# Optimization experiments

Measured on AMD Instinct MI355X. Metric: run time of the kernel, lower is better.

Reference implementation:

```python
import jax, jax.numpy as jnp
import numpy as np

WS, SHIFT, HEADS = 8, 4, 12
B, H0, W0, C, HID = 16, 64, 64, 384, 1536
EPS = 1e-5


def _rel_pos_index():
    # WindowMSA.double_step_seq(2*Ww-1, Wh, 1, Ww), then coords + coords.T, then flip(1)
    seq1 = np.arange(0, (2 * WS - 1) * WS, 2 * WS - 1)
    seq2 = np.arange(0, WS)
    coords = (seq1[:, None] + seq2[None, :]).reshape(1, -1)  # (1, N)
    idx = coords + coords.T                                   # (N, N)
    return np.ascontiguousarray(idx[:, ::-1]).reshape(-1)

REL_IDX = jnp.asarray(_rel_pos_index())


def _attn_mask(Hp, Wp):
    # Swin shift mask: region labels -> per-window pairwise (-100 where regions differ)
    img = np.zeros((Hp, Wp))
    sl = (slice(0, -WS), slice(-WS, -SHIFT), slice(-SHIFT, None))
    cnt = 0
    for hs in sl:
        for ws in sl:
            img[hs, ws] = cnt
            cnt += 1
    mw = img.reshape(Hp // WS, WS, Wp // WS, WS).transpose(0, 2, 1, 3).reshape(-1, WS * WS)
    am = mw[:, None, :] - mw[:, :, None]
    return jnp.asarray(np.where(am != 0, -100.0, 0.0), np.float32)


def _ln(z, g, b):
    m = z.mean(-1, keepdims=True)
    v = ((z - m) ** 2).mean(-1, keepdims=True)
    return (z - m) * jax.lax.rsqrt(v + EPS) * g + b


def _bn(z, g, b):
    # eval-mode BatchNorm2d with running mean=0, var=1
    scale = g * (1.0 / np.sqrt(1.0 + EPS))
    return z * scale[None, :, None, None] + b[None, :, None, None]


def setup_inputs() -> dict:
    key = jax.random.key(0)
    ks = jax.random.split(key, 8)
    p = lambda k, sh: jax.random.normal(k, sh, jnp.float32) * 0.02
    return {
        "x": jax.random.normal(ks[0], (B, H0 * W0, C), jnp.float32),
        "H": H0, "W": W0,
        "ln1_g": jnp.ones((C,), jnp.float32), "ln1_b": jnp.zeros((C,), jnp.float32),
        "qkv_w": p(ks[1], (3 * C, C)), "qkv_b": jnp.zeros((3 * C,), jnp.float32),
        "rpb_table": p(ks[2], ((2 * WS - 1) ** 2, HEADS)),
        "proj_w": p(ks[3], (C, C)), "proj_b": jnp.zeros((C,), jnp.float32),
        "ln2_g": jnp.ones((C,), jnp.float32), "ln2_b": jnp.zeros((C,), jnp.float32),
        "fc1_w": p(ks[4], (HID, C)), "fc1_b": jnp.zeros((HID,), jnp.float32),
        "bn1_g": jnp.ones((HID,), jnp.float32), "bn1_b": jnp.zeros((HID,), jnp.float32),
        "dw_w": p(ks[5], (HID, 1, 3, 3)), "dw_b": jnp.zeros((HID,), jnp.float32),
        "bn2_g": jnp.ones((HID,), jnp.float32), "bn2_b": jnp.zeros((HID,), jnp.float32),
        "fc2_w": p(ks[6], (C, HID)), "fc2_b": jnp.zeros((C,), jnp.float32),
        "bn3_g": jnp.ones((C,), jnp.float32), "bn3_b": jnp.zeros((C,), jnp.float32),
    }


def reference(x, H, W, ln1_g, ln1_b, qkv_w, qkv_b, rpb_table, proj_w, proj_b,
              ln2_g, ln2_b, fc1_w, fc1_b, bn1_g, bn1_b, dw_w, dw_b,
              bn2_g, bn2_b, fc2_w, fc2_b, bn3_g, bn3_b):
    Bx, L, Cx = x.shape
    hd = Cx // HEADS
    # ---------- shifted-window MHSA branch ----------
    h = _ln(x, ln1_g, ln1_b).reshape(Bx, H, W, Cx)
    h = jnp.roll(h, (-SHIFT, -SHIFT), axis=(1, 2))
    nH, nW = H // WS, W // WS
    N = WS * WS
    win = h.reshape(Bx, nH, WS, nW, WS, Cx).transpose(0, 1, 3, 2, 4, 5).reshape(-1, N, Cx)
    qkv = (win @ qkv_w.T + qkv_b).reshape(-1, N, 3, HEADS, hd).transpose(2, 0, 3, 1, 4)
    q, k, v = qkv[0] * (hd ** -0.5), qkv[1], qkv[2]  # (B*nW, heads, N, hd)
    attn = jnp.einsum('whnd,whmd->whnm', q, k)
    bias = rpb_table[REL_IDX].reshape(N, N, HEADS).transpose(2, 0, 1)  # (heads, N, N)
    attn = attn + bias[None]
    mask = _attn_mask(H, W)  # (num_windows, N, N)
    attn = attn.reshape(Bx, nH * nW, HEADS, N, N) + mask[None, :, None]
    attn = jax.nn.softmax(attn.reshape(-1, HEADS, N, N), axis=-1)
    out = jnp.einsum('whnm,whmd->whnd', attn, v).transpose(0, 2, 1, 3).reshape(-1, N, Cx)
    out = out @ proj_w.T + proj_b
    out = out.reshape(Bx, nH, nW, WS, WS, Cx).transpose(0, 1, 3, 2, 4, 5).reshape(Bx, H, W, Cx)
    out = jnp.roll(out, (SHIFT, SHIFT), axis=(1, 2)).reshape(Bx, L, Cx)
    x = x + out
    # ---------- MlpDWBN branch ----------
    h = _ln(x, ln2_g, ln2_b)
    z = h.transpose(0, 2, 1).reshape(Bx, Cx, H, W)
    z = jnp.einsum('oc,bchw->bohw', fc1_w, z) + fc1_b[None, :, None, None]
    z = jax.nn.gelu(_bn(z, bn1_g, bn1_b), approximate=False)
    z = jax.lax.conv_general_dilated(z, dw_w, (1, 1), 'SAME',
                                     feature_group_count=z.shape[1],
                                     dimension_numbers=('NCHW', 'OIHW', 'NCHW'))
    z = z + dw_b[None, :, None, None]
    z = jax.nn.gelu(_bn(z, bn2_g, bn2_b), approximate=False)
    z = jnp.einsum('oc,bchw->bohw', fc2_w, z) + fc2_b[None, :, None, None]
    z = jax.nn.gelu(_bn(z, bn3_g, bn3_b), approximate=False)
    z = z.reshape(Bx, Cx, -1).transpose(0, 2, 1)
    return x + z
```

## Files before the change

### kernel.cpp

```cpp
#include <hip/hip_runtime.h>
#include <cstddef>


#define CCH 384
#define HIDCH 1536

typedef __attribute__((ext_vector_type(8))) short short8;
typedef __attribute__((ext_vector_type(4))) float f32x4;

__device__ __forceinline__ float gelu_exact(float v) {
  return 0.5f * v * (1.0f + erff(v * 0.70710678118654752440f));
}
__device__ __forceinline__ unsigned short f2bf(float f) {
  unsigned u = __builtin_bit_cast(unsigned, f);
  u = (u + 0x7FFF + ((u >> 16) & 1)) >> 16;
  return (unsigned short)u;
}
__device__ __forceinline__ float bf2f(unsigned short s) {
  return __builtin_bit_cast(float, (unsigned)s << 16);
}
__device__ __forceinline__ int region_label(int p) {
  return (p < 56) ? 0 : ((p < 60) ? 1 : 2);
}

__device__ __forceinline__ void gl_lds16(const void* g, void* l) {
  __builtin_amdgcn_global_load_lds(
      (const __attribute__((address_space(1))) unsigned int*)g,
      (__attribute__((address_space(3))) unsigned int*)l, 16, 0, 0);
}

__global__ __launch_bounds__(256) void convw_kernel(
    const float* __restrict__ a, const float* __restrict__ b,
    const float* __restrict__ c, const float* __restrict__ d,
    const float* __restrict__ dww, unsigned short* __restrict__ o,
    float* __restrict__ dwt) {
  const int i = blockIdx.x * 256 + threadIdx.x;
  if (i < 1769472) {
    float v;
    if (i < 442368) v = a[i];
    else if (i < 589824) v = b[i - 442368];
    else if (i < 1179648) v = c[i - 589824];
    else v = d[i - 1179648];
    o[i] = f2bf(v);
  } else if (i < 1769472 + 13824) {
    const int j = i - 1769472;
    const int tap = j / 1536;
    const int ch = j - tap * 1536;
    dwt[j] = dww[ch * 9 + tap];
  }
}

template <int REMAP>
__global__ __launch_bounds__(256) void ln_kernel(const float* __restrict__ x,
                                                 const float* __restrict__ g,
                                                 const float* __restrict__ b,
                                                 unsigned short* __restrict__ y) {
  const int t = blockIdx.x * 4 + (threadIdx.x >> 6);
  const int lane = threadIdx.x & 63;
  size_t src;
  if (REMAP) {
    const int widx = t >> 6;
    const int n = t & 63;
    const int bb = widx >> 6;
    const int wh = (widx >> 3) & 7;
    const int ww = widx & 7;
    const int hp = wh * 8 + (n >> 3);
    const int wp = ww * 8 + (n & 7);
    const int hs = (hp + 4) & 63;
    const int wsrc = (wp + 4) & 63;
    src = (size_t)bb * 4096 + hs * 64 + wsrc;
  } else {
    src = (size_t)t;
  }
  const float* xr = x + src * CCH + lane * 6;
  const float2 p0 = *(const float2*)xr;
  const float2 p1 = *(const float2*)(xr + 2);
  const float2 p2 = *(const float2*)(xr + 4);
  float v[6] = {p0.x, p0.y, p1.x, p1.y, p2.x, p2.y};
  float s = 0.f, s2 = 0.f;
#pragma unroll
  for (int j = 0; j < 6; ++j) {
    s += v[j];
    s2 += v[j] * v[j];
  }
#pragma unroll
  for (int o = 1; o < 64; o <<= 1) {
    s += __shfl_xor(s, o);
    s2 += __shfl_xor(s2, o);
  }
  const float mean = s * (1.0f / 384.0f);
  const float var = s2 * (1.0f / 384.0f) - mean * mean;
  const float rstd = rsqrtf(var + 1e-5f);
  const float2 g0 = *(const float2*)(g + lane * 6);
  const float2 g1 = *(const float2*)(g + lane * 6 + 2);
  const float2 g2 = *(const float2*)(g + lane * 6 + 4);
  const float2 b0 = *(const float2*)(b + lane * 6);
  const float2 b1 = *(const float2*)(b + lane * 6 + 2);
  const float2 b2 = *(const float2*)(b + lane * 6 + 4);
  const float gg[6] = {g0.x, g0.y, g1.x, g1.y, g2.x, g2.y};
  const float bv[6] = {b0.x, b0.y, b1.x, b1.y, b2.x, b2.y};
  unsigned pk[3];
#pragma unroll
  for (int i = 0; i < 3; ++i) {
    const float r0 = (v[2 * i] - mean) * rstd * gg[2 * i] + bv[2 * i];
    const float r1 = (v[2 * i + 1] - mean) * rstd * gg[2 * i + 1] + bv[2 * i + 1];
    pk[i] = (unsigned)f2bf(r0) | ((unsigned)f2bf(r1) << 16);
  }
  unsigned* yo = (unsigned*)(y + (size_t)t * CCH + lane * 6);
  yo[0] = pk[0];
  yo[1] = pk[1];
  yo[2] = pk[2];
}

template <int MODE>
__global__ __launch_bounds__(256) void mfma_gemm(
    const unsigned short* __restrict__ A, const unsigned short* __restrict__ W,
    const float* __restrict__ bias, void* __restrict__ CoutV,
    const float* __restrict__ Xres, const float* __restrict__ bng,
    const float* __restrict__ bnb, int N, int K) {
  __shared__ __align__(16) unsigned short As[128 * 32];
  __shared__ __align__(16) unsigned short Bs[128 * 32];
  const int tid = threadIdx.x;
  const int wave = tid >> 6, lane = tid & 63;
  const int qd = lane >> 4, ln16 = lane & 15;
  const int wm = wave >> 1, wn = wave & 1;
  const int m0 = blockIdx.x * 128;
  const int n0 = blockIdx.y * 128;

  f32x4 acc[4][4];
#pragma unroll
  for (int i = 0; i < 4; ++i)
#pragma unroll
    for (int j = 0; j < 4; ++j) acc[i][j] = (f32x4){0.f, 0.f, 0.f, 0.f};

  const int r = tid >> 2;
  const int ck = (tid & 3) * 8;

  const unsigned short* gA0 = A + (size_t)(m0 + r) * K + ck;
  const unsigned short* gA1 = A + (size_t)(m0 + 64 + r) * K + ck;
  const unsigned short* gB0 = W + (size_t)(n0 + r) * K + ck;
  const unsigned short* gB1 = W + (size_t)(n0 + 64 + r) * K + ck;
  unsigned short* lA0 = As + wave * 512;
  unsigned short* lA1 = As + 2048 + wave * 512;
  unsigned short* lB0 = Bs + wave * 512;
  unsigned short* lB1 = Bs + 2048 + wave * 512;

  for (int k0 = 0; k0 < K; k0 += 32) {
    __syncthreads();
    gl_lds16(gA0 + k0, lA0);
    gl_lds16(gA1 + k0, lA1);
    gl_lds16(gB0 + k0, lB0);
    gl_lds16(gB1 + k0, lB1);
    __syncthreads();
    short8 af[4], bfr[4];
#pragma unroll
    for (int mt = 0; mt < 4; ++mt)
      af[mt] = *(const short8*)&As[(wm * 64 + mt * 16 + ln16) * 32 + qd * 8];
#pragma unroll
    for (int nt = 0; nt < 4; ++nt)
      bfr[nt] = *(const short8*)&Bs[(wn * 64 + nt * 16 + ln16) * 32 + qd * 8];
#pragma unroll
    for (int mt = 0; mt < 4; ++mt)
#pragma unroll
      for (int nt = 0; nt < 4; ++nt)
        acc[mt][nt] = __builtin_amdgcn_mfma_f32_16x16x32_bf16(
            af[mt], bfr[nt], acc[mt][nt], 0, 0, 0);
  }

  const float RSQ = 0.99999500003749969f;
#pragma unroll
  for (int mt = 0; mt < 4; ++mt) {
#pragma unroll
    for (int nt = 0; nt < 4; ++nt) {
      const int col = n0 + wn * 64 + nt * 16 + ln16;
      const int rbase = m0 + wm * 64 + mt * 16 + qd * 4;
#pragma unroll
      for (int rg = 0; rg < 4; ++rg) {
        const int row = rbase + rg;
        const float val = acc[mt][nt][rg] + bias[col];
        if (MODE == 0) {
          ((unsigned short*)CoutV)[(size_t)row * N + col] = f2bf(val);
        } else if (MODE == 1) {
          const int widx = row >> 6, n = row & 63;
          const int bb = widx >> 6, wh = (widx >> 3) & 7, wwi = widx & 7;
          const int hp = wh * 8 + (n >> 3), wp = wwi * 8 + (n & 7);
          const int hh = (hp + 4) & 63, wwp = (wp + 4) & 63;
          const size_t dst = ((size_t)bb * 4096 + hh * 64 + wwp) * CCH + col;
          ((float*)CoutV)[dst] = Xres[dst] + val;
        } else {
          const float vbn = val * (bng[col] * RSQ) + bnb[col];
          const float ge = gelu_exact(vbn);
          if (MODE == 2) {
            ((unsigned short*)CoutV)[(size_t)row * N + col] = f2bf(ge);
          } else {
            float* o = (float*)CoutV + (size_t)row * N + col;
            *o = *o + ge;
          }
        }
      }
    }
  }
}

__global__ __launch_bounds__(256) void attn_kernel(
    const unsigned short* __restrict__ qkv, const float* __restrict__ rpb,
    unsigned short* __restrict__ ao) {
  __shared__ __align__(16) unsigned short Pl[4][64 * 72];
  __shared__ float Inv[4][64];
  const int wloc = blockIdx.x;
  const int wave = threadIdx.x >> 6;
  const int lane = threadIdx.x & 63;
  const int head = blockIdx.y * 4 + wave;
  const int ln16 = lane & 15, qd = lane >> 4;
  const int wpos = wloc & 63;
  const int wh = (wpos >> 3) & 7, ww = wpos & 7;
  const unsigned short* qb = qkv + (size_t)wloc * 64 * 1152 + head * 32;

  short8 aq[4], bk[4];
#pragma unroll
  for (int t = 0; t < 4; ++t) {
    aq[t] = *(const short8*)(qb + (size_t)(t * 16 + ln16) * 1152 + qd * 8);
    bk[t] = *(const short8*)(qb + (size_t)(t * 16 + ln16) * 1152 + 384 + qd * 8);
  }
  short8 av[2][2];
#pragma unroll
  for (int dt = 0; dt < 2; ++dt)
#pragma unroll
    for (int ks = 0; ks < 2; ++ks)
#pragma unroll
      for (int j = 0; j < 8; ++j)
        av[dt][ks][j] = (short)qb[(size_t)(ks * 32 + qd * 8 + j) * 1152 + 768 +
                                  dt * 16 + ln16];

  f32x4 accS[4][4];
#pragma unroll
  for (int i = 0; i < 4; ++i)
#pragma unroll
    for (int j = 0; j < 4; ++j) accS[i][j] = (f32x4){0.f, 0.f, 0.f, 0.f};
#pragma unroll
  for (int mt = 0; mt < 4; ++mt)
#pragma unroll
    for (int nt = 0; nt < 4; ++nt)
      accS[mt][nt] = __builtin_amdgcn_mfma_f32_16x16x32_bf16(
          aq[mt], bk[nt], accS[mt][nt], 0, 0, 0);

  int cmv[4], rlm[4];
#pragma unroll
  for (int nt = 0; nt < 4; ++nt) {
    const int m = nt * 16 + ln16;
    const int mf = 63 - m;
    cmv[nt] = 15 * (mf >> 3) + (mf & 7);
    rlm[nt] =
        region_label(wh * 8 + (m >> 3)) * 3 + region_label(ww * 8 + (m & 7));
  }
  const float scale = 0.17677669529663687f;
  unsigned short* pw = &Pl[wave][0];
#pragma unroll
  for (int mt = 0; mt < 4; ++mt) {
#pragma unroll
    for (int rg = 0; rg < 4; ++rg) {
      const int n = mt * 16 + qd * 4 + rg;
      const int cn = 15 * (n >> 3) + (n & 7);
      const int rln =
          region_label(wh * 8 + (n >> 3)) * 3 + region_label(ww * 8 + (n & 7));
      float vv[4];
#pragma unroll
      for (int nt = 0; nt < 4; ++nt) {
        float sv = accS[mt][nt][rg] * scale + rpb[(cn + cmv[nt]) * 12 + head];
        if (rln != rlm[nt]) sv -= 100.f;
        vv[nt] = sv;
      }
      float mx = fmaxf(fmaxf(vv[0], vv[1]), fmaxf(vv[2], vv[3]));
      mx = fmaxf(mx, __shfl_xor(mx, 1));
      mx = fmaxf(mx, __shfl_xor(mx, 2));
      mx = fmaxf(mx, __shfl_xor(mx, 4));
      mx = fmaxf(mx, __shfl_xor(mx, 8));
      float sum = 0.f;
#pragma unroll
      for (int nt = 0; nt < 4; ++nt) {
        vv[nt] = __expf(vv[nt] - mx);
        sum += vv[nt];
      }
      sum += __shfl_xor(sum, 1);
      sum += __shfl_xor(sum, 2);
      sum += __shfl_xor(sum, 4);
      sum += __shfl_xor(sum, 8);
      if (ln16 == 0) Inv[wave][n] = 1.0f / sum;
#pragma unroll
      for (int nt = 0; nt < 4; ++nt)
        pw[n * 72 + nt * 16 + ln16] = f2bf(vv[nt]);
    }
  }

  f32x4 accO[2][4];
#pragma unroll
  for (int i = 0; i < 2; ++i)
#pragma unroll
    for (int j = 0; j < 4; ++j) accO[i][j] = (f32x4){0.f, 0.f, 0.f, 0.f};
#pragma unroll
  for (int ks = 0; ks < 2; ++ks) {
    short8 pb[4];
#pragma unroll
    for (int ntile = 0; ntile < 4; ++ntile)
      pb[ntile] =
          *(const short8*)&pw[(ntile * 16 + ln16) * 72 + ks * 32 + qd * 8];
#pragma unroll
    for (int dt = 0; dt < 2; ++dt)
#pragma unroll
      for (int ntile = 0; ntile < 4; ++ntile)
        accO[dt][ntile] = __builtin_amdgcn_mfma_f32_16x16x32_bf16(
            av[dt][ks], pb[ntile], accO[dt][ntile], 0, 0, 0);
  }

  float invn[4];
#pragma unroll
  for (int ntile = 0; ntile < 4; ++ntile)
    invn[ntile] = Inv[wave][ntile * 16 + ln16];
#pragma unroll
  for (int dt = 0; dt < 2; ++dt) {
#pragma unroll
    for (int ntile = 0; ntile < 4; ++ntile) {
      const int tok = ntile * 16 + ln16;
      const int d0 = dt * 16 + qd * 4;
      uint2 st;
      st.x = (unsigned)f2bf(accO[dt][ntile][0] * invn[ntile]) |
             ((unsigned)f2bf(accO[dt][ntile][1] * invn[ntile]) << 16);
      st.y = (unsigned)f2bf(accO[dt][ntile][2] * invn[ntile]) |
             ((unsigned)f2bf(accO[dt][ntile][3] * invn[ntile]) << 16);
      *(uint2*)&ao[((size_t)wloc * 64 + tok) * CCH + head * 32 + d0] = st;
    }
  }
}

__global__ __launch_bounds__(256) void dw_kernel(
    const unsigned short* __restrict__ z1, const float* __restrict__ dwt,
    const float* __restrict__ dwb, const float* __restrict__ bn2g,
    const float* __restrict__ bn2b, unsigned short* __restrict__ z2) {
  const int g = blockIdx.x * 256 + threadIdx.x;
  const int pix = g / 192;
  const int cg = g - pix * 192;
  const int c0 = cg * 8;
  const int p = pix & 4095;
  const int h = p >> 6, w = p & 63;
  const unsigned short* zb = z1 + (size_t)(pix >> 12) * 4096 * HIDCH;

  float a[8];
  {
    const float4 b0 = *(const float4*)&dwb[c0];
    const float4 b1 = *(const float4*)&dwb[c0 + 4];
    a[0] = b0.x; a[1] = b0.y; a[2] = b0.z; a[3] = b0.w;
    a[4] = b1.x; a[5] = b1.y; a[6] = b1.z; a[7] = b1.w;
  }
#pragma unroll
  for (int dh = -1; dh <= 1; ++dh) {
    const int hh = h + dh;
    if (hh < 0 || hh > 63) continue;
#pragma unroll
    for (int dx = -1; dx <= 1; ++dx) {
      const int wn = w + dx;
      if (wn < 0 || wn > 63) continue;
      const int tap = (dh + 1) * 3 + (dx + 1);
      const int4 zv = *(const int4*)&zb[((size_t)hh * 64 + wn) * HIDCH + c0];
      const float* wp = &dwt[tap * HIDCH + c0];
      const float4 w0 = *(const float4*)wp;
      const float4 w1 = *(const float4*)(wp + 4);
      a[0] += bf2f((unsigned short)(zv.x & 0xFFFF)) * w0.x;
      a[1] += bf2f((unsigned short)(((unsigned)zv.x) >> 16)) * w0.y;
      a[2] += bf2f((unsigned short)(zv.y & 0xFFFF)) * w0.z;
      a[3] += bf2f((unsigned short)(((unsigned)zv.y) >> 16)) * w0.w;
      a[4] += bf2f((unsigned short)(zv.z & 0xFFFF)) * w1.x;
      a[5] += bf2f((unsigned short)(((unsigned)zv.z) >> 16)) * w1.y;
      a[6] += bf2f((unsigned short)(zv.w & 0xFFFF)) * w1.z;
      a[7] += bf2f((unsigned short)(((unsigned)zv.w) >> 16)) * w1.w;
    }
  }
  const float RSQ = 0.99999500003749969f;
  const float4 g0 = *(const float4*)&bn2g[c0];
  const float4 g1 = *(const float4*)&bn2g[c0 + 4];
  const float4 bb0 = *(const float4*)&bn2b[c0];
  const float4 bb1 = *(const float4*)&bn2b[c0 + 4];
  const float gs[8] = {g0.x, g0.y, g0.z, g0.w, g1.x, g1.y, g1.z, g1.w};
  const float bs[8] = {bb0.x, bb0.y, bb0.z, bb0.w, bb1.x, bb1.y, bb1.z, bb1.w};
  unsigned pk[4];
#pragma unroll
  for (int i = 0; i < 4; ++i) {
    const float v0 = gelu_exact(a[2 * i] * (gs[2 * i] * RSQ) + bs[2 * i]);
    const float v1 =
        gelu_exact(a[2 * i + 1] * (gs[2 * i + 1] * RSQ) + bs[2 * i + 1]);
    pk[i] = (unsigned)f2bf(v0) | ((unsigned)f2bf(v1) << 16);
  }
  int4 st;
  st.x = pk[0]; st.y = pk[1]; st.z = pk[2]; st.w = pk[3];
  *(int4*)&z2[(size_t)pix * HIDCH + c0] = st;
}

extern "C" void kernel_launch(void* const* d_in, const int* in_sizes, int n_in,
                              void* d_out, int out_size, void* d_ws,
                              size_t ws_size, hipStream_t stream) {
  const float* x = (const float*)d_in[0];
  const float* ln1_g = (const float*)d_in[3];
  const float* ln1_b = (const float*)d_in[4];
  const float* qkv_w = (const float*)d_in[5];
  const float* qkv_b = (const float*)d_in[6];
  const float* rpb = (const float*)d_in[7];
  const float* proj_w = (const float*)d_in[8];
  const float* proj_b = (const float*)d_in[9];
  const float* ln2_g = (const float*)d_in[10];
  const float* ln2_b = (const float*)d_in[11];
  const float* fc1_w = (const float*)d_in[12];
  const float* fc1_b = (const float*)d_in[13];
  const float* bn1_g = (const float*)d_in[14];
  const float* bn1_b = (const float*)d_in[15];
  const float* dw_w = (const float*)d_in[16];
  const float* dw_b = (const float*)d_in[17];
  const float* bn2_g = (const float*)d_in[18];
  const float* bn2_b = (const float*)d_in[19];
  const float* fc2_w = (const float*)d_in[20];
  const float* fc2_b = (const float*)d_in[21];
  const float* bn3_g = (const float*)d_in[22];
  const float* bn3_b = (const float*)d_in[23];
  float* out = (float*)d_out;

  char* ws = (char*)d_ws;
  unsigned short* wsA = (unsigned short*)ws;
  unsigned short* wsAO = (unsigned short*)(ws + 50331648);
  unsigned short* wsQ = (unsigned short*)(ws + 100663296);
  unsigned short* wbf = (unsigned short*)(ws + 150994944);
  float* dwt = (float*)(ws + 154533888);
  unsigned short* w_qkv = wbf;
  unsigned short* w_proj = wbf + 442368;
  unsigned short* w_fc1 = wbf + 589824;
  unsigned short* w_fc2 = wbf + 1179648;

  convw_kernel<<<6966, 256, 0, stream>>>(qkv_w, proj_w, fc1_w, fc2_w, dw_w,
                                         wbf, dwt);
  ln_kernel<1><<<16384, 256, 0, stream>>>(x, ln1_g, ln1_b, wsA);
  for (int cb = 0; cb < 4; ++cb) {
    mfma_gemm<0><<<dim3(128, 9), 256, 0, stream>>>(
        wsA + (size_t)cb * 16384 * CCH, w_qkv, qkv_b, wsQ, nullptr, nullptr,
        nullptr, 1152, CCH);
    attn_kernel<<<dim3(256, 3), 256, 0, stream>>>(
        wsQ, rpb, wsAO + (size_t)cb * 16384 * CCH);
  }
  mfma_gemm<1><<<dim3(512, 3), 256, 0, stream>>>(wsAO, w_proj, proj_b, out, x,
                                                 nullptr, nullptr, CCH, CCH);
  ln_kernel<0><<<16384, 256, 0, stream>>>(out, ln2_g, ln2_b, wsA);
  for (int cb = 0; cb < 4; ++cb) {
    mfma_gemm<2><<<dim3(128, 12), 256, 0, stream>>>(
        wsA + (size_t)cb * 16384 * CCH, w_fc1, fc1_b, wsAO, nullptr, bn1_g,
        bn1_b, HIDCH, CCH);
    dw_kernel<<<12288, 256, 0, stream>>>(wsAO, dwt, dw_b, bn2_g, bn2_b, wsQ);
    mfma_gemm<3><<<dim3(128, 3), 256, 0, stream>>>(
        wsQ, w_fc2, fc2_b, out + (size_t)cb * 16384 * CCH, nullptr, bn3_g,
        bn3_b, CCH, HIDCH);
  }
}
```

Before: 1.160 ms.

## Double-buffer GEMM LDS tiles and XOR-swizzle K chunks to cut bank conflicts

The MFMA GEMM now keeps two LDS buffers for the A and B tiles and prefetches the next K tile with direct global-to-LDS loads while computing the current one. Explicit vmcnt waits and two barriers per iteration replace the old load-then-sync pattern. Global column offsets are XOR-swizzled by row, and fragment reads use the matching swizzle, so the LDS reads should hit fewer banks at once. In exchange it doubles the LDS footprint, which may reduce occupancy, and it depends on the hand-written waitcnt counts being correct.

New measurement: 1.122 ms. -3.3%, faster.

```diff
diff --git a/kernel.cpp b/kernel.cpp
--- a/kernel.cpp
+++ b/kernel.cpp
@@ -118,8 +118,8 @@
     const float* __restrict__ bias, void* __restrict__ CoutV,
     const float* __restrict__ Xres, const float* __restrict__ bng,
     const float* __restrict__ bnb, int N, int K) {
-  __shared__ __align__(16) unsigned short As[128 * 32];
-  __shared__ __align__(16) unsigned short Bs[128 * 32];
+  __shared__ __align__(16) unsigned short As[2][128 * 32];
+  __shared__ __align__(16) unsigned short Bs[2][128 * 32];
   const int tid = threadIdx.x;
   const int wave = tid >> 6, lane = tid & 63;
   const int qd = lane >> 4, ln16 = lane & 15;
@@ -134,50 +134,66 @@
     for (int j = 0; j < 4; ++j) acc[i][j] = (f32x4){0.f, 0.f, 0.f, 0.f};
 
   const int r = tid >> 2;
-  const int ck = (tid & 3) * 8;
-
-  const unsigned short* gA0 = A + (size_t)(m0 + r) * K + ck;
-  const unsigned short* gA1 = A + (size_t)(m0 + 64 + r) * K + ck;
-  const unsigned short* gB0 = W + (size_t)(n0 + r) * K + ck;
-  const unsigned short* gB1 = W + (size_t)(n0 + 64 + r) * K + ck;
-  unsigned short* lA0 = As + wave * 512;
-  unsigned short* lA1 = As + 2048 + wave * 512;
-  unsigned short* lB0 = Bs + wave * 512;
-  unsigned short* lB1 = Bs + 2048 + wave * 512;
-
-  for (int k0 = 0; k0 < K; k0 += 32) {
-    __syncthreads();
-    gl_lds16(gA0 + k0, lA0);
-    gl_lds16(gA1 + k0, lA1);
-    gl_lds16(gB0 + k0, lB0);
-    gl_lds16(gB1 + k0, lB1);
-    __syncthreads();
+  const int cks = ((tid & 3) ^ ((tid >> 3) & 3)) * 8;
+
+  const unsigned short* gA0 = A + (size_t)(m0 + r) * K + cks;
+  const unsigned short* gA1 = A + (size_t)(m0 + 64 + r) * K + cks;
+  const unsigned short* gB0 = W + (size_t)(n0 + r) * K + cks;
+  const unsigned short* gB1 = W + (size_t)(n0 + 64 + r) * K + cks;
+  const int lofs = wave * 512;
+
+  const int nt = K >> 5;
+  gl_lds16(gA0, &As[0][lofs]);
+  gl_lds16(gA1, &As[0][2048 + lofs]);
+  gl_lds16(gB0, &Bs[0][lofs]);
+  gl_lds16(gB1, &Bs[0][2048 + lofs]);
+
+  const int sA = (qd ^ ((ln16 >> 1) & 3)) * 8;
+
+  int cur = 0;
+  for (int t = 0; t < nt; ++t) {
+    __builtin_amdgcn_s_barrier();
+    __builtin_amdgcn_sched_barrier(0);
+    if (t + 1 < nt) {
+      const int k1 = (t + 1) * 32;
+      const int nb = cur ^ 1;
+      gl_lds16(gA0 + k1, &As[nb][lofs]);
+      gl_lds16(gA1 + k1, &As[nb][2048 + lofs]);
+      gl_lds16(gB0 + k1, &Bs[nb][lofs]);
+      gl_lds16(gB1 + k1, &Bs[nb][2048 + lofs]);
+      asm volatile("s_waitcnt vmcnt(4)" ::: "memory");
+    } else {
+      asm volatile("s_waitcnt vmcnt(0)" ::: "memory");
+    }
+    __builtin_amdgcn_s_barrier();
+    __builtin_amdgcn_sched_barrier(0);
     short8 af[4], bfr[4];
 #pragma unroll
     for (int mt = 0; mt < 4; ++mt)
-      af[mt] = *(const short8*)&As[(wm * 64 + mt * 16 + ln16) * 32 + qd * 8];
-#pragma unroll
-    for (int nt = 0; nt < 4; ++nt)
-      bfr[nt] = *(const short8*)&Bs[(wn * 64 + nt * 16 + ln16) * 32 + qd * 8];
+      af[mt] = *(const short8*)&As[cur][(wm * 64 + mt * 16 + ln16) * 32 + sA];
+#pragma unroll
+    for (int nt2 = 0; nt2 < 4; ++nt2)
+      bfr[nt2] = *(const short8*)&Bs[cur][(wn * 64 + nt2 * 16 + ln16) * 32 + sA];
 #pragma unroll
     for (int mt = 0; mt < 4; ++mt)
 #pragma unroll
-      for (int nt = 0; nt < 4; ++nt)
-        acc[mt][nt] = __builtin_amdgcn_mfma_f32_16x16x32_bf16(
-            af[mt], bfr[nt], acc[mt][nt], 0, 0, 0);
+      for (int nt2 = 0; nt2 < 4; ++nt2)
+        acc[mt][nt2] = __builtin_amdgcn_mfma_f32_16x16x32_bf16(
+            af[mt], bfr[nt2], acc[mt][nt2], 0, 0, 0);
+    cur ^= 1;
   }
 
   const float RSQ = 0.99999500003749969f;
 #pragma unroll
   for (int mt = 0; mt < 4; ++mt) {
 #pragma unroll
-    for (int nt = 0; nt < 4; ++nt) {
-      const int col = n0 + wn * 64 + nt * 16 + ln16;
+    for (int nt2 = 0; nt2 < 4; ++nt2) {
+      const int col = n0 + wn * 64 + nt2 * 16 + ln16;
       const int rbase = m0 + wm * 64 + mt * 16 + qd * 4;
 #pragma unroll
       for (int rg = 0; rg < 4; ++rg) {
         const int row = rbase + rg;
-        const float val = acc[mt][nt][rg] + bias[col];
+        const float val = acc[mt][nt2][rg] + bias[col];
         if (MODE == 0) {
           ((unsigned short*)CoutV)[(size_t)row * N + col] = f2bf(val);
         } else if (MODE == 1) {
```
